# Optimization experiments

Hardware: AMD Instinct MI355X
Metric: run time of the kernel (lower is better)

## Reference

```python
import jax, jax.numpy as jnp
import numpy as np

T, B, COV, H, L = 512, 256, 128, 512, 2
N_DIST_PARAMS = 2  # lnormal


def setup_inputs() -> dict:
    key = jax.random.key(0)
    ks = jax.random.split(key, 20)
    d = {}
    d["x"] = jax.random.normal(ks[0], (T, B, COV + 1), jnp.float32)
    lengths = jax.random.randint(ks[1], (B,), 2, T + 1)
    lengths = -jnp.sort(-lengths)  # packed sequences: descending lengths
    lengths = lengths.at[0].set(T)  # ensure max length == T
    d["lengths"] = lengths
    d["h0"] = jax.random.normal(ks[2], (L, B, H), jnp.float32)
    s = 1.0 / np.sqrt(H)
    in_dims = [COV + 1, H]
    for l in range(L):
        d[f"Wih{l}"] = jax.random.uniform(ks[3 + 4 * l], (3 * H, in_dims[l]), jnp.float32, -s, s)
        d[f"Whh{l}"] = jax.random.uniform(ks[4 + 4 * l], (3 * H, H), jnp.float32, -s, s)
        d[f"bih{l}"] = jax.random.uniform(ks[5 + 4 * l], (3 * H,), jnp.float32, -s, s)
        d[f"bhh{l}"] = jax.random.uniform(ks[6 + 4 * l], (3 * H,), jnp.float32, -s, s)
    sc = 1.0 / np.sqrt(H + 1)
    d["W_cov"] = jax.random.uniform(ks[11], (COV, H + 1), jnp.float32, -sc, sc)
    d["b_cov"] = jax.random.uniform(ks[12], (COV,), jnp.float32, -sc, sc)
    sp = 1.0 / np.sqrt(L * H)
    d["W_par"] = jax.random.uniform(ks[13], (N_DIST_PARAMS, L * H), jnp.float32, -sp, sp)
    d["b_par"] = jax.random.uniform(ks[14], (N_DIST_PARAMS,), jnp.float32, -sp, sp)
    return d


def gru_layer(x, h0, lengths, Wih, Whh, bih, bhh):
    # x: [T, B, D]; h0: [B, H]. PyTorch GRU gate math, masked for ragged lengths
    gi = jnp.einsum('tbd,gd->tbg', x, Wih) + bih  # [T, B, 3H], one big GEMM
    tt = jnp.arange(x.shape[0])

    def step(h, inp):
        gi_t, t = inp
        gh = h @ Whh.T + bhh
        i_r, i_z, i_n = jnp.split(gi_t, 3, axis=-1)
        h_r, h_z, h_n = jnp.split(gh, 3, axis=-1)
        r = jax.nn.sigmoid(i_r + h_r)
        z = jax.nn.sigmoid(i_z + h_z)
        n = jnp.tanh(i_n + r * h_n)
        h_new = (1.0 - z) * n + z * h
        valid = (t < lengths)[:, None]
        h = jnp.where(valid, h_new, h)          # freeze carry past length
        out = jnp.where(valid, h_new, 0.0)       # pad_packed_sequence zero-pads
        return h, out

    h_last, outs = jax.lax.scan(step, h0, (gi, tt))
    return outs, h_last


def reference(x, lengths, h0, Wih0, Whh0, bih0, bhh0, Wih1, Whh1, bih1, bhh1, W_cov, b_cov, W_par, b_par):
    o0, hl0 = gru_layer(x, h0[0], lengths, Wih0, Whh0, bih0, bhh0)
    o1, hl1 = gru_layer(o0, h0[1], lengths, Wih1, Whh1, bih1, bhh1)
    hs = jnp.transpose(o1, (1, 0, 2))  # [B, T, H]
    times = x[:, :, 0].T               # [B, T]
    hwt = jnp.concatenate([hs, times[..., None]], axis=-1)  # [B, T, H+1]
    Tm = x.shape[0]
    # batched masked matmul replacing per-(batch, timestep) GEMV loop
    preds = jnp.einsum('bth,ch->btc', hwt[:, :Tm - 1], W_cov) + b_cov  # [B, T-1, COV]
    mask = (jnp.arange(Tm - 1)[None, :] < (lengths - 1)[:, None])[..., None]
    preds = jnp.where(mask, preds, 0.0)
    # original writes COV values into a COV+1 wide zero buffer; last channel stays 0
    preds = jnp.concatenate([preds, jnp.zeros(preds.shape[:2] + (1,), preds.dtype)], axis=-1)
    last_hidden = jnp.stack([hl0, hl1])                      # [L, B, H]
    last_flat = jnp.reshape(last_hidden, (last_hidden.shape[1], -1))  # torch .view semantics
    dist_params = last_flat @ W_par.T + b_par
    return preds, jnp.exp(-dist_params)
```

## Files before the change

kernel.cpp:

```cpp
#include <hip/hip_runtime.h>


typedef unsigned short u16;
typedef unsigned long long u64;
typedef __attribute__((ext_vector_type(8))) short short8;
typedef short8 bf16x8;
typedef __attribute__((ext_vector_type(4))) float f32x4;

#define T_DIM 512
#define B_DIM 256
#define H_DIM 512
#define G3H   1536
#define BT    131072
#define XPK   192
#define PRED_ELEMS 16875264

#define GLD16(gp, lp) __builtin_amdgcn_global_load_lds( \
    (const __attribute__((address_space(1))) void*)(gp), \
    (__attribute__((address_space(3))) void*)(lp), 16, 0, 0)

__device__ __forceinline__ u16 f2bf(float f) {
    union { float f; unsigned i; } v; v.f = f;
    unsigned i = v.i;
    return (u16)((i + 0x7FFFu + ((i >> 16) & 1u)) >> 16);
}
__device__ __forceinline__ float bf2f(u16 u) {
    union { unsigned i; float f; } v; v.i = ((unsigned)u) << 16; return v.f;
}
__device__ __forceinline__ float sigm(float x) { return 1.f / (1.f + __expf(-x)); }
__device__ __forceinline__ float tanh_f(float x) {
    float ax = fabsf(x);
    float e = __expf(-2.f * ax);
    float t = (1.f - e) / (1.f + e);
    return x < 0.f ? -t : t;
}
__device__ __forceinline__ bf16x8 aload16(const u16* p) {
    union { bf16x8 v; u64 q[2]; } r;
    const u64* qp = (const u64*)p;
    r.q[0] = __hip_atomic_load(qp + 0, __ATOMIC_RELAXED, __HIP_MEMORY_SCOPE_AGENT);
    r.q[1] = __hip_atomic_load(qp + 1, __ATOMIC_RELAXED, __HIP_MEMORY_SCOPE_AGENT);
    return r.v;
}

__global__ void prep_kernel(const float* __restrict__ Wih0, const float* __restrict__ Wih1,
                            const float* __restrict__ Whh0, const float* __restrict__ Whh1,
                            const float* __restrict__ h0,   const float* __restrict__ Wcov,
                            u16* __restrict__ wih0b, u16* __restrict__ wih1b,
                            u16* __restrict__ whh0b, u16* __restrict__ whh1b,
                            u16* __restrict__ h0bf,  u16* __restrict__ wcovb,
                            float* __restrict__ wlastf, unsigned* __restrict__ ctr) {
    const int gid = blockIdx.x * 256 + threadIdx.x;
    const int gsz = gridDim.x * 256;
    for (int i = gid; i < 2048; i += gsz) ctr[i] = 0u;
    for (int i = gid; i < 128; i += gsz) wlastf[i] = Wcov[i * 513 + 512];
    for (int i = gid; i < 128 * 512; i += gsz) {
        int r = i >> 9, c = i & 511;
        wcovb[i] = f2bf(Wcov[r * 513 + c]);
    }
    for (int i = gid; i < 512 * 512; i += gsz) h0bf[i] = f2bf(h0[i]);
    for (int i = gid; i < 1536 * 192; i += gsz) {
        int r = i / 192, c = i - r * 192;
        wih0b[i] = f2bf(c < 129 ? Wih0[r * 129 + c] : 0.f);
    }
    for (int i = gid; i < 1536 * 512; i += gsz) wih1b[i] = f2bf(Wih1[i]);
    for (int i = gid; i < 1536 * 512; i += gsz) whh0b[i] = f2bf(Whh0[i]);
    for (int i = gid; i < 1536 * 512; i += gsz) whh1b[i] = f2bf(Whh1[i]);
}

__global__ void cvt_pad_x_kernel(const float* __restrict__ src,
                                 u16* __restrict__ dst, int rows) {
    const int n = rows * 192;
    for (int idx = blockIdx.x * blockDim.x + threadIdx.x; idx < n;
         idx += gridDim.x * blockDim.x) {
        const int row = idx / 192, col = idx - row * 192;
        float v = (col < 129) ? src[(size_t)row * 129 + col] : 0.f;
        dst[idx] = f2bf(v);
    }
}

__global__ __launch_bounds__(256) void gemm_bias_kernel(
    const u16* __restrict__ A, int lda, const u16* __restrict__ B, int ldb,
    const float* __restrict__ bias, u16* __restrict__ C, int ldc, int K) {
    __shared__ __attribute__((aligned(16))) u16 Sh[2][16384];
    const int tid = threadIdx.x, lane = tid & 63, w = tid >> 6;
    const int m0 = blockIdx.y * 128, n0 = blockIdx.x * 128;
    const int r0 = (w & 1) * 64, c0 = (w >> 1) * 64;
    const int am = lane & 15, aq = lane >> 4;
    const int l8 = lane >> 3, lc = lane & 7;
    const int swz = (lc ^ l8) << 3;
    const int NT = K >> 6;
    f32x4 acc[4][4] = {};
#pragma unroll
    for (int s = 0; s < 4; ++s) {
        const int i = w * 4 + s, row = i * 8 + l8;
        GLD16(A + (size_t)(m0 + row) * lda + swz, &Sh[0][i * 512]);
        GLD16(B + (size_t)(n0 + row) * ldb + swz, &Sh[0][8192 + i * 512]);
    }
    __syncthreads();
    int cur = 0;
    for (int kt = 0; kt < NT; ++kt) {
        if (kt + 1 < NT) {
            const int kb = (kt + 1) << 6;
#pragma unroll
            for (int s = 0; s < 4; ++s) {
                const int i = w * 4 + s, row = i * 8 + l8;
                GLD16(A + (size_t)(m0 + row) * lda + kb + swz,
                      &Sh[cur ^ 1][i * 512]);
                GLD16(B + (size_t)(n0 + row) * ldb + kb + swz,
                      &Sh[cur ^ 1][8192 + i * 512]);
            }
        }
        const u16* Ash = &Sh[cur][0];
        const u16* Bsh = &Sh[cur][8192];
#pragma unroll
        for (int ks = 0; ks < 2; ++ks) {
            bf16x8 a[4], bb[4];
#pragma unroll
            for (int f = 0; f < 4; ++f) {
                const int ar = r0 + f * 16 + am;
                a[f] = *(short8*)&Ash[ar * 64 + (((ks * 4 + aq) ^ (ar & 7)) << 3)];
            }
#pragma unroll
            for (int f = 0; f < 4; ++f) {
                const int br = c0 + f * 16 + am;
                bb[f] = *(short8*)&Bsh[br * 64 + (((ks * 4 + aq) ^ (br & 7)) << 3)];
            }
#pragma unroll
            for (int fi = 0; fi < 4; ++fi)
#pragma unroll
                for (int fj = 0; fj < 4; ++fj)
                    acc[fi][fj] = __builtin_amdgcn_mfma_f32_16x16x32_bf16(
                        a[fi], bb[fj], acc[fi][fj], 0, 0, 0);
        }
        __syncthreads();
        cur ^= 1;
    }
    u16* Ep = &Sh[0][0];
#pragma unroll
    for (int fj = 0; fj < 4; ++fj) {
        const int col = c0 + fj * 16 + am;
        const float bia = bias[n0 + col];
#pragma unroll
        for (int fi = 0; fi < 4; ++fi)
#pragma unroll
            for (int r = 0; r < 4; ++r)
                Ep[(r0 + fi * 16 + aq * 4 + r) * 128 + col] =
                    f2bf(acc[fi][fj][r] + bia);
    }
    __syncthreads();
#pragma unroll
    for (int s = 0; s < 8; ++s) {
        const int chunk = tid + s * 256;
        const int row = chunk >> 4, qo = (chunk & 15) * 8;
        *(short8*)(C + (size_t)(m0 + row) * ldc + n0 + qo) =
            *(short8*)&Ep[row * 128 + qo];
    }
}

__global__ __launch_bounds__(256, 2) void scan_gru_kernel(
    const u16* __restrict__ gi,
    const u16* __restrict__ Whh,
    const float* __restrict__ bhh,
    const int* __restrict__ lengths,
    const float* __restrict__ h0l,
    const u16* __restrict__ h0bfl,
    u16* __restrict__ o,
    u16* __restrict__ hbf,
    float* __restrict__ hlast,
    unsigned* __restrict__ ctr,
    int t0, int TC, unsigned base) {
    __shared__ __attribute__((aligned(16))) u16 Wl[48 * 520];
    __shared__ __attribute__((aligned(16))) float P[4 * 3 * 256];
    __shared__ __attribute__((aligned(16))) float bhhf[48];
    const int tid = threadIdx.x, lane = tid & 63, w = tid >> 6;
    const int n0 = blockIdx.x * 16, b0 = blockIdx.y * 16;
#pragma unroll
    for (int it = 0; it < 12; ++it) {
        int f = it * 2048 + tid * 8;
        int j = f >> 9, k = f & 511;
        *(short8*)&Wl[j * 520 + k] =
            *(const short8*)(Whh + ((size_t)((j >> 4) * 512 + n0 + (j & 15))) * 512 + k);
    }
    if (tid < 48) bhhf[tid] = bhh[(tid >> 4) * 512 + n0 + (tid & 15)];
    const int m = tid >> 4, c = tid & 15;
    const int b = b0 + m, col = n0 + c;
    float h = (t0 == 0) ? h0l[(size_t)b * 512 + col]
                        : hlast[(size_t)b * 512 + col];
    const int len = lengths[b];
    const int am = lane & 15, aq = lane >> 4;
    unsigned* flg = ctr + blockIdx.y * 32;
    const unsigned* myprod = flg + w * 8;
    size_t gib = (size_t)b * (size_t)G3H + n0 + c;
    float gr = bf2f(gi[gib]), gz = bf2f(gi[gib + 512]), gn = bf2f(gi[gib + 1024]);
    __syncthreads();
    for (int tl = 0; tl < TC; ++tl) {
        const int t = t0 + tl;
        if (tl > 0) {
            const unsigned tgt = base + (unsigned)tl;
            if (lane < 8) {
                const unsigned* fp = myprod + lane;
                while (__hip_atomic_load(fp, __ATOMIC_RELAXED,
                                         __HIP_MEMORY_SCOPE_AGENT) < tgt)
                    __builtin_amdgcn_s_sleep(1);
            }
            asm volatile("" ::: "memory");
        }
        const u16* Asrc = (t == 0) ? h0bfl : (hbf + (size_t)((t - 1) & 1) * BT);
        bf16x8 a4[4];
#pragma unroll
        for (int kb = 0; kb < 4; ++kb)
            a4[kb] = aload16(Asrc + (size_t)(b0 + am) * 512 + w * 128 + kb * 32 + aq * 8);
        f32x4 ar = {}, az = {}, an = {};
#pragma unroll
        for (int kb = 0; kb < 4; ++kb) {
            const int k = w * 128 + kb * 32 + aq * 8;
            bf16x8 wr = *(short8*)&Wl[(0 + am) * 520 + k];
            bf16x8 wz = *(short8*)&Wl[(16 + am) * 520 + k];
            bf16x8 wn = *(short8*)&Wl[(32 + am) * 520 + k];
            ar = __builtin_amdgcn_mfma_f32_16x16x32_bf16(a4[kb], wr, ar, 0, 0, 0);
            az = __builtin_amdgcn_mfma_f32_16x16x32_bf16(a4[kb], wz, az, 0, 0, 0);
            an = __builtin_amdgcn_mfma_f32_16x16x32_bf16(a4[kb], wn, an, 0, 0, 0);
        }
#pragma unroll
        for (int r = 0; r < 4; ++r) {
            P[(w * 3 + 0) * 256 + (aq * 4 + r) * 16 + am] = ar[r];
            P[(w * 3 + 1) * 256 + (aq * 4 + r) * 16 + am] = az[r];
            P[(w * 3 + 2) * 256 + (aq * 4 + r) * 16 + am] = an[r];
        }
        __syncthreads();
        float Cr = bhhf[c], Cz = bhhf[16 + c], Cn = bhhf[32 + c];
#pragma unroll
        for (int w2 = 0; w2 < 4; ++w2) {
            Cr += P[(w2 * 3 + 0) * 256 + tid];
            Cz += P[(w2 * 3 + 1) * 256 + tid];
            Cn += P[(w2 * 3 + 2) * 256 + tid];
        }
        float r_ = sigm(gr + Cr);
        float z_ = sigm(gz + Cz);
        float n_ = tanh_f(gn + r_ * Cn);
        float hnew = (1.f - z_) * n_ + z_ * h;
        bool valid = t < len;
        h = valid ? hnew : h;
        if (tl < TC - 1) {
            unsigned hb = (unsigned)f2bf(h);
            unsigned part = hb | ((unsigned)__shfl_down((int)hb, 1) << 16);
            unsigned hi2 = (unsigned)__shfl_down((int)part, 2);
            if ((lane & 3) == 0) {
                u64 q = (u64)part | ((u64)hi2 << 32);
                const int mrow = w * 4 + (lane >> 4);
                const int cg = lane & 15;
                __hip_atomic_store(
                    (u64*)(hbf + (size_t)(t & 1) * BT + (size_t)(b0 + mrow) * 512 + n0 + cg),
                    q, __ATOMIC_RELAXED, __HIP_MEMORY_SCOPE_AGENT);
            }
            __syncthreads();
            if (tid == 0)
                __hip_atomic_store(flg + blockIdx.x, base + (unsigned)tl + 1u,
                                   __ATOMIC_RELAXED, __HIP_MEMORY_SCOPE_AGENT);
            o[((size_t)tl * 256 + b) * 512 + col] = f2bf(valid ? hnew : 0.f);
            const size_t gib2 = ((size_t)(tl + 1) * 256 + b) * (size_t)G3H + n0 + c;
            gr = bf2f(gi[gib2]); gz = bf2f(gi[gib2 + 512]); gn = bf2f(gi[gib2 + 1024]);
        } else {
            o[((size_t)tl * 256 + b) * 512 + col] = f2bf(valid ? hnew : 0.f);
            hbf[(size_t)(t & 1) * BT + (size_t)b * 512 + col] = f2bf(h);
            hlast[(size_t)b * 512 + col] = h;
        }
    }
}

__global__ __launch_bounds__(256) void preds_kernel(
    const u16* __restrict__ o1c, const u16* __restrict__ WcovBf,
    const float* __restrict__ wlastf, const float* __restrict__ bcov,
    const float* __restrict__ x, const int* __restrict__ lengths,
    float* __restrict__ out, int t0) {
    __shared__ __attribute__((aligned(16))) u16 Sh[2][16384];
    const int tid = threadIdx.x, lane = tid & 63, w = tid >> 6;
    const int m0 = blockIdx.x * 128;
    const int r0 = (w & 1) * 64, c0 = (w >> 1) * 64;
    const int am = lane & 15, aq = lane >> 4;
    const int l8 = lane >> 3, lc = lane & 7;
    const int swz = (lc ^ l8) << 3;
    f32x4 acc[4][4] = {};
#pragma unroll
    for (int s = 0; s < 4; ++s) {
        const int i = w * 4 + s, row = i * 8 + l8;
        GLD16(o1c + (size_t)(m0 + row) * 512 + swz, &Sh[0][i * 512]);
        GLD16(WcovBf + (size_t)row * 512 + swz, &Sh[0][8192 + i * 512]);
    }
    __syncthreads();
    int cur = 0;
    for (int kt = 0; kt < 8; ++kt) {
        if (kt + 1 < 8) {
            const int kb = (kt + 1) << 6;
#pragma unroll
            for (int s = 0; s < 4; ++s) {
                const int i = w * 4 + s, row = i * 8 + l8;
                GLD16(o1c + (size_t)(m0 + row) * 512 + kb + swz,
                      &Sh[cur ^ 1][i * 512]);
                GLD16(WcovBf + (size_t)row * 512 + kb + swz,
                      &Sh[cur ^ 1][8192 + i * 512]);
            }
        }
        const u16* Ash = &Sh[cur][0];
        const u16* Bsh = &Sh[cur][8192];
#pragma unroll
        for (int ks = 0; ks < 2; ++ks) {
            bf16x8 a[4], bb[4];
#pragma unroll
            for (int f = 0; f < 4; ++f) {
                const int ar2 = r0 + f * 16 + am;
                a[f] = *(short8*)&Ash[ar2 * 64 + (((ks * 4 + aq) ^ (ar2 & 7)) << 3)];
            }
#pragma unroll
            for (int f = 0; f < 4; ++f) {
                const int br = c0 + f * 16 + am;
                bb[f] = *(short8*)&Bsh[br * 64 + (((ks * 4 + aq) ^ (br & 7)) << 3)];
            }
#pragma unroll
            for (int fi = 0; fi < 4; ++fi)
#pragma unroll
                for (int fj = 0; fj < 4; ++fj)
                    acc[fi][fj] = __builtin_amdgcn_mfma_f32_16x16x32_bf16(
                        a[fi], bb[fj], acc[fi][fj], 0, 0, 0);
        }
        __syncthreads();
        cur ^= 1;
    }
    const int tl = m0 >> 8;
    const int t = t0 + tl;
    if (t < 511) {
#pragma unroll
        for (int fj = 0; fj < 4; ++fj) {
            const int cc = c0 + fj * 16 + am;
            const float bc = bcov[cc], wl = wlastf[cc];
#pragma unroll
            for (int fi = 0; fi < 4; ++fi) {
#pragma unroll
                for (int r = 0; r < 4; ++r) {
                    const int row = m0 + r0 + fi * 16 + aq * 4 + r;
                    const int b = row & 255;
                    const bool valid = t < lengths[b] - 1;
                    const float tim = x[(size_t)t * (256 * 129) + b * 129];
                    out[(size_t)b * (511 * 129) + (size_t)t * 129 + cc] =
                        valid ? acc[fi][fj][r] + bc + tim * wl : 0.f;
                }
            }
        }
        if (tid < 128)
            out[(size_t)((m0 & 255) + tid) * (511 * 129) + (size_t)t * 129 + 128] = 0.f;
    }
}

__global__ void dist_kernel(const float* __restrict__ hl0,
                            const float* __restrict__ hl1,
                            const float* __restrict__ Wpar,
                            const float* __restrict__ bpar, float* __restrict__ out) {
    const int w = threadIdx.x >> 6, lane = threadIdx.x & 63;
    const float bp0 = bpar[0], bp1 = bpar[1];
    for (int rr = 0; rr < 8; ++rr) {
        const int i = (blockIdx.x * 4 + w) * 8 + rr;
        const int l = i >> 7, bb = (2 * i) & 255;
        const float* base = (l ? hl1 : hl0) + (size_t)bb * 512;
        float a0 = 0.f, a1 = 0.f;
#pragma unroll
        for (int cc = 0; cc < 16; ++cc) {
            const int k = cc * 64 + lane;
            const float v = base[k];
            a0 += v * Wpar[k];
            a1 += v * Wpar[1024 + k];
        }
#pragma unroll
        for (int off = 32; off; off >>= 1) {
            a0 += __shfl_down(a0, off);
            a1 += __shfl_down(a1, off);
        }
        if (lane == 0) {
            out[PRED_ELEMS + i * 2 + 0] = __expf(-(a0 + bp0));
            out[PRED_ELEMS + i * 2 + 1] = __expf(-(a1 + bp1));
        }
    }
}

extern "C" void kernel_launch(void* const* d_in, const int* in_sizes, int n_in,
                              void* d_out, int out_size, void* d_ws, size_t ws_size,
                              hipStream_t stream) {
    const float* x    = (const float*)d_in[0];
    const int* lens   = (const int*)d_in[1];
    const float* h0   = (const float*)d_in[2];
    const float* Wih0 = (const float*)d_in[3];
    const float* Whh0 = (const float*)d_in[4];
    const float* bih0 = (const float*)d_in[5];
    const float* bhh0 = (const float*)d_in[6];
    const float* Wih1 = (const float*)d_in[7];
    const float* Whh1 = (const float*)d_in[8];
    const float* bih1 = (const float*)d_in[9];
    const float* bhh1 = (const float*)d_in[10];
    const float* Wcov = (const float*)d_in[11];
    const float* bcov = (const float*)d_in[12];
    const float* Wpar = (const float*)d_in[13];
    const float* bpar = (const float*)d_in[14];
    float* out = (float*)d_out;
    char* wsb = (char*)d_ws;

    size_t off = 0;
    auto take = [&](size_t bytes) -> size_t {
        size_t r = off; off += (bytes + 255) & ~(size_t)255; return r;
    };
    const size_t oCtr   = take(8192);
    const size_t oHl0   = take((size_t)BT * 4);
    const size_t oHl1   = take((size_t)BT * 4);
    const size_t oHbf0  = take((size_t)2 * BT * 2);
    const size_t oHbf1  = take((size_t)2 * BT * 2);
    const size_t oH0bf  = take((size_t)2 * BT * 2);
    const size_t oWih0b = take((size_t)G3H * XPK * 2);
    const size_t oWih1b = take((size_t)G3H * 512 * 2);
    const size_t oWhh0b = take((size_t)G3H * 512 * 2);
    const size_t oWhh1b = take((size_t)G3H * 512 * 2);
    const size_t oWcovb = take((size_t)128 * 512 * 2);
    const size_t oWlast = take(512);
    const size_t fixed = off;

    const size_t per = (size_t)256 * XPK * 2 + (size_t)256 * G3H * 2 +
                       2 * (size_t)256 * 512 * 2 + 2048;
    const size_t remain = ws_size > fixed ? ws_size - fixed : 0;
    int TC = 1;
    const int cands[10] = {512, 256, 128, 64, 32, 16, 8, 4, 2, 1};
    for (int i = 0; i < 10; ++i)
        if ((size_t)cands[i] * per <= remain) { TC = cands[i]; break; }

    const size_t oXbf = take((size_t)TC * 256 * XPK * 2);
    const size_t oGi  = take((size_t)TC * 256 * G3H * 2);
    const size_t oO0  = take((size_t)TC * 256 * 512 * 2);
    const size_t oO1  = take((size_t)TC * 256 * 512 * 2);

    unsigned* ctr = (unsigned*)(wsb + oCtr);
    float* hl0  = (float*)(wsb + oHl0);
    float* hl1  = (float*)(wsb + oHl1);
    u16* hbf0   = (u16*)(wsb + oHbf0);
    u16* hbf1   = (u16*)(wsb + oHbf1);
    u16* h0bf   = (u16*)(wsb + oH0bf);
    u16* wih0b  = (u16*)(wsb + oWih0b);
    u16* wih1b  = (u16*)(wsb + oWih1b);
    u16* whh0b  = (u16*)(wsb + oWhh0b);
    u16* whh1b  = (u16*)(wsb + oWhh1b);
    u16* wcovb  = (u16*)(wsb + oWcovb);
    float* wlastf = (float*)(wsb + oWlast);
    u16* xbfc   = (u16*)(wsb + oXbf);
    u16* gic    = (u16*)(wsb + oGi);
    u16* o0c    = (u16*)(wsb + oO0);
    u16* o1c    = (u16*)(wsb + oO1);

    prep_kernel<<<1024, 256, 0, stream>>>(Wih0, Wih1, Whh0, Whh1, h0, Wcov,
                                          wih0b, wih1b, whh0b, whh1b, h0bf,
                                          wcovb, wlastf, ctr);

    unsigned base = 0;
    for (int t0 = 0; t0 < T_DIM; t0 += TC) {
        int n = TC * 256 * XPK;
        int pg = (n + 255) / 256; if (pg > 2048) pg = 2048;
        cvt_pad_x_kernel<<<pg, 256, 0, stream>>>(
            x + (size_t)t0 * 256 * 129, xbfc, TC * 256);
        gemm_bias_kernel<<<dim3(12, TC * 2), 256, 0, stream>>>(
            xbfc, XPK, wih0b, XPK, bih0, gic, G3H, XPK);
        scan_gru_kernel<<<dim3(32, 16), 256, 0, stream>>>(
            gic, whh0b, bhh0, lens, h0, h0bf, o0c, hbf0, hl0,
            ctr, t0, TC, base);
        gemm_bias_kernel<<<dim3(12, TC * 2), 256, 0, stream>>>(
            o0c, H_DIM, wih1b, H_DIM, bih1, gic, G3H, H_DIM);
        scan_gru_kernel<<<dim3(32, 16), 256, 0, stream>>>(
            gic, whh1b, bhh1, lens, h0 + (size_t)BT, h0bf + (size_t)BT,
            o1c, hbf1, hl1, ctr + 1024, t0, TC, base);
        preds_kernel<<<dim3(TC * 2), 256, 0, stream>>>(
            o1c, wcovb, wlastf, bcov, x, lens, out, t0);
        base += (unsigned)(TC - 1);
    }
    dist_kernel<<<8, 256, 0, stream>>>(hl0, hl1, Wpar, bpar, out);
}
```

Baseline: 4.899 ms.

## Replace flag-counter inter-block sync with NaN-sentinel polling on hidden-state data

The recurrent scan no longer publishes per-step progress through atomic counter flags followed by a block barrier. Each block now writes its bf16 hidden state straight into the per-step output buffer, and consumers spin on the loaded values until none equal a NaN sentinel. The output buffers are pre-filled with the sentinel, and the gate partial-sum LDS buffer is double-buffered so the second per-step __syncthreads can be dropped. This is meant to shorten the serial per-timestep critical path, at the cost of extra sentinel fill traffic and reliance on the fact that real hidden values never encode as that NaN pattern.

```diff
diff --git a/kernel.cpp b/kernel.cpp
--- a/kernel.cpp
+++ b/kernel.cpp
@@ -14,6 +14,7 @@
 #define BT    131072
 #define XPK   192
 #define PRED_ELEMS 16875264
+#define SENT  0x7FC0u
 
 #define GLD16(gp, lp) __builtin_amdgcn_global_load_lds( \
     (const __attribute__((address_space(1))) void*)(gp), \
@@ -41,6 +42,16 @@
     r.q[1] = __hip_atomic_load(qp + 1, __ATOMIC_RELAXED, __HIP_MEMORY_SCOPE_AGENT);
     return r.v;
 }
+__device__ __forceinline__ unsigned chk8(bf16x8 v) {
+    union { bf16x8 v; unsigned d[4]; } u; u.v = v;
+    unsigned b = 0;
+#pragma unroll
+    for (int i = 0; i < 4; ++i) {
+        unsigned d = u.d[i] ^ 0x7FC07FC0u;
+        b |= (unsigned)((d & 0xFFFFu) == 0u) | (unsigned)((d >> 16) == 0u);
+    }
+    return b;
+}
 
 __global__ void prep_kernel(const float* __restrict__ Wih0, const float* __restrict__ Wih1,
                             const float* __restrict__ Whh0, const float* __restrict__ Whh1,
@@ -48,10 +59,10 @@
                             u16* __restrict__ wih0b, u16* __restrict__ wih1b,
                             u16* __restrict__ whh0b, u16* __restrict__ whh1b,
                             u16* __restrict__ h0bf,  u16* __restrict__ wcovb,
-                            float* __restrict__ wlastf, unsigned* __restrict__ ctr) {
+                            float* __restrict__ wlastf,
+                            u16* __restrict__ o0c, u16* __restrict__ o1c, int TC) {
     const int gid = blockIdx.x * 256 + threadIdx.x;
     const int gsz = gridDim.x * 256;
-    for (int i = gid; i < 2048; i += gsz) ctr[i] = 0u;
     for (int i = gid; i < 128; i += gsz) wlastf[i] = Wcov[i * 513 + 512];
     for (int i = gid; i < 128 * 512; i += gsz) {
         int r = i >> 9, c = i & 511;
@@ -65,6 +76,21 @@
     for (int i = gid; i < 1536 * 512; i += gsz) wih1b[i] = f2bf(Wih1[i]);
     for (int i = gid; i < 1536 * 512; i += gsz) whh0b[i] = f2bf(Whh0[i]);
     for (int i = gid; i < 1536 * 512; i += gsz) whh1b[i] = f2bf(Whh1[i]);
+    const u64 SQ = 0x7FC07FC07FC07FC0ULL;
+    const size_t nq = (size_t)TC * BT / 4;
+    u64* p0 = (u64*)o0c;
+    u64* p1 = (u64*)o1c;
+    for (size_t i = gid; i < nq; i += gsz) p0[i] = SQ;
+    for (size_t i = gid; i < nq; i += gsz) p1[i] = SQ;
+}
+
+__global__ void sentinel_kernel(u16* __restrict__ buf, int TC) {
+    const u64 SQ = 0x7FC07FC07FC07FC0ULL;
+    const size_t nq = (size_t)TC * BT / 4;
+    u64* p = (u64*)buf;
+    const size_t gid = blockIdx.x * 256 + threadIdx.x;
+    const size_t gsz = (size_t)gridDim.x * 256;
+    for (size_t i = gid; i < nq; i += gsz) p[i] = SQ;
 }
 
 __global__ void cvt_pad_x_kernel(const float* __restrict__ src,
@@ -165,12 +191,11 @@
     const float* __restrict__ h0l,
     const u16* __restrict__ h0bfl,
     u16* __restrict__ o,
-    u16* __restrict__ hbf,
+    u16* __restrict__ hcarry,
     float* __restrict__ hlast,
-    unsigned* __restrict__ ctr,
-    int t0, int TC, unsigned base) {
+    int t0, int TC) {
     __shared__ __attribute__((aligned(16))) u16 Wl[48 * 520];
-    __shared__ __attribute__((aligned(16))) float P[4 * 3 * 256];
+    __shared__ __attribute__((aligned(16))) float P[2][12 * 256];
     __shared__ __attribute__((aligned(16))) float bhhf[48];
     const int tid = threadIdx.x, lane = tid & 63, w = tid >> 6;
     const int n0 = blockIdx.x * 16, b0 = blockIdx.y * 16;
@@ -188,28 +213,33 @@
                         : hlast[(size_t)b * 512 + col];
     const int len = lengths[b];
     const int am = lane & 15, aq = lane >> 4;
-    unsigned* flg = ctr + blockIdx.y * 32;
-    const unsigned* myprod = flg + w * 8;
     size_t gib = (size_t)b * (size_t)G3H + n0 + c;
     float gr = bf2f(gi[gib]), gz = bf2f(gi[gib + 512]), gn = bf2f(gi[gib + 1024]);
     __syncthreads();
+    int pb = 0;
     for (int tl = 0; tl < TC; ++tl) {
         const int t = t0 + tl;
-        if (tl > 0) {
-            const unsigned tgt = base + (unsigned)tl;
-            if (lane < 8) {
-                const unsigned* fp = myprod + lane;
-                while (__hip_atomic_load(fp, __ATOMIC_RELAXED,
-                                         __HIP_MEMORY_SCOPE_AGENT) < tgt)
-                    __builtin_amdgcn_s_sleep(1);
-            }
-            asm volatile("" ::: "memory");
-        }
-        const u16* Asrc = (t == 0) ? h0bfl : (hbf + (size_t)((t - 1) & 1) * BT);
-        bf16x8 a4[4];
-#pragma unroll
-        for (int kb = 0; kb < 4; ++kb)
-            a4[kb] = aload16(Asrc + (size_t)(b0 + am) * 512 + w * 128 + kb * 32 + aq * 8);
+        const u16* Asrc = (tl == 0) ? ((t0 == 0) ? h0bfl : hcarry)
+                                    : (o + (size_t)(tl - 1) * BT);
+        const u16* arow = Asrc + (size_t)(b0 + am) * 512 + w * 128 + aq * 8;
+        bf16x8 av[4];
+        if (tl == 0) {
+            av[0] = aload16(arow);      av[1] = aload16(arow + 32);
+            av[2] = aload16(arow + 64); av[3] = aload16(arow + 96);
+        } else {
+            for (;;) {
+                av[0] = aload16(arow);
+                if (!__any((int)chk8(av[0]))) break;
+                __builtin_amdgcn_s_sleep(1);
+            }
+            for (;;) {
+                av[1] = aload16(arow + 32);
+                av[2] = aload16(arow + 64);
+                av[3] = aload16(arow + 96);
+                if (!__any((int)(chk8(av[1]) | chk8(av[2]) | chk8(av[3])))) break;
+                __builtin_amdgcn_s_sleep(1);
+            }
+        }
         f32x4 ar = {}, az = {}, an = {};
 #pragma unroll
         for (int kb = 0; kb < 4; ++kb) {
@@ -217,54 +247,48 @@
             bf16x8 wr = *(short8*)&Wl[(0 + am) * 520 + k];
             bf16x8 wz = *(short8*)&Wl[(16 + am) * 520 + k];
             bf16x8 wn = *(short8*)&Wl[(32 + am) * 520 + k];
-            ar = __builtin_amdgcn_mfma_f32_16x16x32_bf16(a4[kb], wr, ar, 0, 0, 0);
-            az = __builtin_amdgcn_mfma_f32_16x16x32_bf16(a4[kb], wz, az, 0, 0, 0);
-            an = __builtin_amdgcn_mfma_f32_16x16x32_bf16(a4[kb], wn, an, 0, 0, 0);
+            ar = __builtin_amdgcn_mfma_f32_16x16x32_bf16(av[kb], wr, ar, 0, 0, 0);
+            az = __builtin_amdgcn_mfma_f32_16x16x32_bf16(av[kb], wz, az, 0, 0, 0);
+            an = __builtin_amdgcn_mfma_f32_16x16x32_bf16(av[kb], wn, an, 0, 0, 0);
         }
 #pragma unroll
         for (int r = 0; r < 4; ++r) {
-            P[(w * 3 + 0) * 256 + (aq * 4 + r) * 16 + am] = ar[r];
-            P[(w * 3 + 1) * 256 + (aq * 4 + r) * 16 + am] = az[r];
-            P[(w * 3 + 2) * 256 + (aq * 4 + r) * 16 + am] = an[r];
+            P[pb][(w * 3 + 0) * 256 + (aq * 4 + r) * 16 + am] = ar[r];
+            P[pb][(w * 3 + 1) * 256 + (aq * 4 + r) * 16 + am] = az[r];
+            P[pb][(w * 3 + 2) * 256 + (aq * 4 + r) * 16 + am] = an[r];
         }
         __syncthreads();
         float Cr = bhhf[c], Cz = bhhf[16 + c], Cn = bhhf[32 + c];
 #pragma unroll
         for (int w2 = 0; w2 < 4; ++w2) {
-            Cr += P[(w2 * 3 + 0) * 256 + tid];
-            Cz += P[(w2 * 3 + 1) * 256 + tid];
-            Cn += P[(w2 * 3 + 2) * 256 + tid];
+            Cr += P[pb][(w2 * 3 + 0) * 256 + tid];
+            Cz += P[pb][(w2 * 3 + 1) * 256 + tid];
+            Cn += P[pb][(w2 * 3 + 2) * 256 + tid];
         }
         float r_ = sigm(gr + Cr);
         float z_ = sigm(gz + Cz);
         float n_ = tanh_f(gn + r_ * Cn);
         float hnew = (1.f - z_) * n_ + z_ * h;
-        bool valid = t < len;
-        h = valid ? hnew : h;
+        h = (t < len) ? hnew : h;
+        unsigned hb = (unsigned)f2bf(h);
+        unsigned part = hb | ((unsigned)__shfl_down((int)hb, 1) << 16);
+        unsigned hi2 = (unsigned)__shfl_down((int)part, 2);
+        if ((lane & 3) == 0) {
+            u64 q = (u64)part | ((u64)hi2 << 32);
+            const int mrow = w * 4 + (lane >> 4);
+            const int cg = lane & 15;
+            __hip_atomic_store(
+                (u64*)(o + (size_t)tl * BT + (size_t)(b0 + mrow) * 512 + n0 + cg),
+                q, __ATOMIC_RELAXED, __HIP_MEMORY_SCOPE_AGENT);
+        }
         if (tl < TC - 1) {
-            unsigned hb = (unsigned)f2bf(h);
-            unsigned part = hb | ((unsigned)__shfl_down((int)hb, 1) << 16);
-            unsigned hi2 = (unsigned)__shfl_down((int)part, 2);
-            if ((lane & 3) == 0) {
-                u64 q = (u64)part | ((u64)hi2 << 32);
-                const int mrow = w * 4 + (lane >> 4);
-                const int cg = lane & 15;
-                __hip_atomic_store(
-                    (u64*)(hbf + (size_t)(t & 1) * BT + (size_t)(b0 + mrow) * 512 + n0 + cg),
-                    q, __ATOMIC_RELAXED, __HIP_MEMORY_SCOPE_AGENT);
-            }
-            __syncthreads();
-            if (tid == 0)
-                __hip_atomic_store(flg + blockIdx.x, base + (unsigned)tl + 1u,
-                                   __ATOMIC_RELAXED, __HIP_MEMORY_SCOPE_AGENT);
-            o[((size_t)tl * 256 + b) * 512 + col] = f2bf(valid ? hnew : 0.f);
             const size_t gib2 = ((size_t)(tl + 1) * 256 + b) * (size_t)G3H + n0 + c;
             gr = bf2f(gi[gib2]); gz = bf2f(gi[gib2 + 512]); gn = bf2f(gi[gib2 + 1024]);
         } else {
-            o[((size_t)tl * 256 + b) * 512 + col] = f2bf(valid ? hnew : 0.f);
-            hbf[(size_t)(t & 1) * BT + (size_t)b * 512 + col] = f2bf(h);
+            hcarry[(size_t)b * 512 + col] = f2bf(h);
             hlast[(size_t)b * 512 + col] = h;
         }
+        pb ^= 1;
     }
 }
 
@@ -406,11 +430,10 @@
     auto take = [&](size_t bytes) -> size_t {
         size_t r = off; off += (bytes + 255) & ~(size_t)255; return r;
     };
-    const size_t oCtr   = take(8192);
     const size_t oHl0   = take((size_t)BT * 4);
     const size_t oHl1   = take((size_t)BT * 4);
-    const size_t oHbf0  = take((size_t)2 * BT * 2);
-    const size_t oHbf1  = take((size_t)2 * BT * 2);
+    const size_t oHc0   = take((size_t)BT * 2);
+    const size_t oHc1   = take((size_t)BT * 2);
     const size_t oH0bf  = take((size_t)2 * BT * 2);
     const size_t oWih0b = take((size_t)G3H * XPK * 2);
     const size_t oWih1b = take((size_t)G3H * 512 * 2);
@@ -433,11 +456,10 @@
     const size_t oO0  = take((size_t)TC * 256 * 512 * 2);
     const size_t oO1  = take((size_t)TC * 256 * 512 * 2);
 
-    unsigned* ctr = (unsigned*)(wsb + oCtr);
     float* hl0  = (float*)(wsb + oHl0);
     float* hl1  = (float*)(wsb + oHl1);
-    u16* hbf0   = (u16*)(wsb + oHbf0);
-    u16* hbf1   = (u16*)(wsb + oHbf1);
+    u16* hcar0  = (u16*)(wsb + oHc0);
+    u16* hcar1  = (u16*)(wsb + oHc1);
     u16* h0bf   = (u16*)(wsb + oH0bf);
     u16* wih0b  = (u16*)(wsb + oWih0b);
     u16* wih1b  = (u16*)(wsb + oWih1b);
@@ -452,9 +474,8 @@
 
     prep_kernel<<<1024, 256, 0, stream>>>(Wih0, Wih1, Whh0, Whh1, h0, Wcov,
                                           wih0b, wih1b, whh0b, whh1b, h0bf,
-                                          wcovb, wlastf, ctr);
-
-    unsigned base = 0;
+                                          wcovb, wlastf, o0c, o1c, TC);
+
     for (int t0 = 0; t0 < T_DIM; t0 += TC) {
         int n = TC * 256 * XPK;
         int pg = (n + 255) / 256; if (pg > 2048) pg = 2048;
@@ -462,17 +483,19 @@
             x + (size_t)t0 * 256 * 129, xbfc, TC * 256);
         gemm_bias_kernel<<<dim3(12, TC * 2), 256, 0, stream>>>(
             xbfc, XPK, wih0b, XPK, bih0, gic, G3H, XPK);
+        if (t0 > 0)
+            sentinel_kernel<<<2048, 256, 0, stream>>>(o0c, TC);
         scan_gru_kernel<<<dim3(32, 16), 256, 0, stream>>>(
-            gic, whh0b, bhh0, lens, h0, h0bf, o0c, hbf0, hl0,
-            ctr, t0, TC, base);
+            gic, whh0b, bhh0, lens, h0, h0bf, o0c, hcar0, hl0, t0, TC);
         gemm_bias_kernel<<<dim3(12, TC * 2), 256, 0, stream>>>(
             o0c, H_DIM, wih1b, H_DIM, bih1, gic, G3H, H_DIM);
+        if (t0 > 0)
+            sentinel_kernel<<<2048, 256, 0, stream>>>(o1c, TC);
         scan_gru_kernel<<<dim3(32, 16), 256, 0, stream>>>(
             gic, whh1b, bhh1, lens, h0 + (size_t)BT, h0bf + (size_t)BT,
-            o1c, hbf1, hl1, ctr + 1024, t0, TC, base);
+            o1c, hcar1, hl1, t0, TC);
         preds_kernel<<<dim3(TC * 2), 256, 0, stream>>>(
             o1c, wcovb, wlastf, bcov, x, lens, out, t0);
-        base += (unsigned)(TC - 1);
     }
     dist_kernel<<<8, 256, 0, stream>>>(hl0, hl1, Wpar, bpar, out);
 }
```

Result: faster. 4.531 ms (-7.5%).
